# Kernel tuning notes

Measured on AMD Instinct MI355X. Metric: run time of the kernel, lower is better.

The kernel has to match this reference:

```python
import jax, jax.numpy as jnp
import numpy as np

N_HEAD, D_MODEL, D_HEAD = 16, 1024, 64
SEQ, BATCH = 1024, 8
SCALE = 1.0 / (D_HEAD ** 0.5)
LN_EPS = 1e-5


def setup_inputs() -> dict:
    key = jax.random.key(0)
    ks = jax.random.split(key, 16)
    dk = N_HEAD * D_HEAD  # == D_MODEL
    init_qkv = 1.0 / np.sqrt(D_MODEL)
    init_out = 1.0 / np.sqrt(dk)
    u = lambda k, shp, lo, hi: jax.random.uniform(k, shp, jnp.float32, lo, hi)
    inp = {
        'dec_inp': jax.random.normal(ks[0], (SEQ, BATCH, D_MODEL), jnp.float32),
        'attn_mask': jnp.triu(jnp.ones((SEQ, SEQ), dtype=bool), k=1),  # causal
        'query_mean': u(ks[1], (dk, D_MODEL), -init_qkv, init_qkv),
        'key_mean': u(ks[2], (dk, D_MODEL), -init_qkv, init_qkv),
        'value_mean': u(ks[3], (dk, D_MODEL), -init_qkv, init_qkv),
        'query_std': u(ks[4], (dk, D_MODEL), 2 * np.log(init_qkv), np.log(init_qkv)),
        'key_std': u(ks[5], (dk, D_MODEL), 2 * np.log(init_qkv), np.log(init_qkv)),
        'value_std': u(ks[6], (dk, D_MODEL), 2 * np.log(init_qkv), np.log(init_qkv)),
        'output_mean': u(ks[7], (D_MODEL, dk), -init_out, init_out),
        'output_std': u(ks[8], (D_MODEL, dk), 2 * np.log(init_out), np.log(init_out)),
        'ln_gamma': jnp.ones((D_MODEL,), jnp.float32),
        'ln_beta': jnp.zeros((D_MODEL,), jnp.float32),
        # per-forward reparameterization noise (training mode)
        'eps_q': jax.random.normal(ks[9], (dk, D_MODEL), jnp.float32),
        'eps_k': jax.random.normal(ks[10], (dk, D_MODEL), jnp.float32),
        'eps_v': jax.random.normal(ks[11], (dk, D_MODEL), jnp.float32),
        'eps_o': jax.random.normal(ks[12], (D_MODEL, dk), jnp.float32),
    }
    return inp


def _forward(dec_inp, query_mean, key_mean, value_mean, query_std, key_std,
             value_std, output_mean, output_std, ln_gamma, ln_beta,
             eps_q, eps_k, eps_v, eps_o, attn_mask):
    S, B, _ = dec_inp.shape
    # Bayesian weight sampling: w = mean + eps * exp(std)
    qw = query_mean + eps_q * jnp.exp(query_std)
    kw = key_mean + eps_k * jnp.exp(key_std)
    vw = value_mean + eps_v * jnp.exp(value_std)
    # NOTE: original code (bug kept for faithfulness) builds the output weight
    # from value_mean + output_diff, not output_mean.
    ow = value_mean + eps_o * jnp.exp(output_std)

    head_q = (dec_inp @ qw.T).reshape(S, B, N_HEAD, D_HEAD)
    head_k = (dec_inp @ kw.T).reshape(S, B, N_HEAD, D_HEAD)
    head_v = (dec_inp @ vw.T).reshape(S, B, N_HEAD, D_HEAD)

    score = jnp.einsum('ibnd,jbnd->ijbn', head_q, head_k) * SCALE
    score = jnp.where(attn_mask[:, :, None, None], -jnp.inf, score)
    prob = jax.nn.softmax(score, axis=1)  # softmax over j (key) axis
    attn_vec = jnp.einsum('ijbn,jbnd->ibnd', prob, head_v).reshape(S, B, N_HEAD * D_HEAD)

    attn_out = attn_vec @ ow.T
    x = dec_inp + attn_out
    mu = jnp.mean(x, axis=-1, keepdims=True)
    var = jnp.var(x, axis=-1, keepdims=True)
    output = (x - mu) * jax.lax.rsqrt(var + LN_EPS) * ln_gamma + ln_beta

    theta_mean = jnp.concatenate([query_mean, key_mean, value_mean, output_mean.T], -1)
    theta_std = jnp.concatenate([query_std, key_std, value_std, output_std.T], -1)
    kl = jnp.mean(theta_mean ** 2 - theta_std * 2.0 + jnp.exp(theta_std * 2.0)) / 2.0
    return output, kl


def reference(dec_inp, attn_mask, query_mean, key_mean, value_mean, query_std,
              key_std, value_std, output_mean, output_std, ln_gamma, ln_beta,
              eps_q, eps_k, eps_v, eps_o):
    return _forward(dec_inp, query_mean, key_mean, value_mean, query_std,
                    key_std, value_std, output_mean, output_std, ln_gamma,
                    ln_beta, eps_q, eps_k, eps_v, eps_o, attn_mask)
```

## Files before the change

kernel.cpp:

```cpp
#include <hip/hip_runtime.h>

typedef _Float16 f16x8 __attribute__((ext_vector_type(8)));
typedef _Float16 f16x4 __attribute__((ext_vector_type(4)));
typedef float    f32x4 __attribute__((ext_vector_type(4)));

static __device__ __forceinline__ f32x4 mfma16(f16x8 a, f16x8 b, f32x4 c) {
    return __builtin_amdgcn_mfma_f32_16x16x32_f16(a, b, c, 0, 0, 0);
}

static __device__ __forceinline__ void gload_lds16(const _Float16* g, _Float16* lds) {
    __builtin_amdgcn_global_load_lds(
        (const __attribute__((address_space(1))) unsigned int*)g,
        (__attribute__((address_space(3))) unsigned int*)lds, 16, 0, 0);
}

__global__ __launch_bounds__(256) void k_prep(
    const float* __restrict__ qm, const float* __restrict__ km, const float* __restrict__ vm,
    const float* __restrict__ qs, const float* __restrict__ ks, const float* __restrict__ vs,
    const float* __restrict__ om, const float* __restrict__ os,
    const float* __restrict__ eq, const float* __restrict__ ek,
    const float* __restrict__ ev, const float* __restrict__ eo,
    _Float16* __restrict__ wq, _Float16* __restrict__ wk,
    _Float16* __restrict__ wv, _Float16* __restrict__ wo,
    float* __restrict__ part,
    const float* __restrict__ dec, _Float16* __restrict__ xh)
{
    if (blockIdx.x >= 4096) {
        int i = ((blockIdx.x - 4096) * 256 + threadIdx.x) * 4;
        float4 v = *(const float4*)&dec[i];
        f16x4 hv;
        hv[0] = (_Float16)v.x; hv[1] = (_Float16)v.y;
        hv[2] = (_Float16)v.z; hv[3] = (_Float16)v.w;
        *(f16x4*)&xh[i] = hv;
        return;
    }
    int i = blockIdx.x * 256 + threadIdx.x;
    float aqm = qm[i], akm = km[i], avm = vm[i];
    float aqs = qs[i], aks = ks[i], avs = vs[i];
    float aom = om[i], aos = os[i];
    wq[i] = (_Float16)(aqm + eq[i] * __expf(aqs));
    wk[i] = (_Float16)(akm + ek[i] * __expf(aks));
    wv[i] = (_Float16)(avm + ev[i] * __expf(avs));
    wo[i] = (_Float16)(avm + eo[i] * __expf(aos));
    float t = aqm*aqm - 2.f*aqs + __expf(2.f*aqs)
            + akm*akm - 2.f*aks + __expf(2.f*aks)
            + avm*avm - 2.f*avs + __expf(2.f*avs)
            + aom*aom - 2.f*aos + __expf(2.f*aos);
    #pragma unroll
    for (int m = 1; m < 64; m <<= 1) t += __shfl_xor(t, m, 64);
    __shared__ float red[4];
    int w = threadIdx.x >> 6, lane = threadIdx.x & 63;
    if (lane == 0) red[w] = t;
    __syncthreads();
    if (threadIdx.x == 0) part[blockIdx.x] = red[0] + red[1] + red[2] + red[3];
}

__global__ __launch_bounds__(256) void k_gemm(
    const _Float16* __restrict__ A, const _Float16* __restrict__ B0,
    _Float16* __restrict__ C0, const float* __restrict__ resid,
    float* __restrict__ xout, int mode)
{
    __shared__ __align__(16) _Float16 As[128 * 64];
    __shared__ __align__(16) _Float16 Bs[128 * 64];
    const int K = 1024, N = 1024;
    const _Float16* Bp = B0 + (size_t)blockIdx.z * 1048576u;
    _Float16* Cp = C0 + (size_t)blockIdx.z * 8388608u;
    int flat = blockIdx.y * 8 + blockIdx.x;
    int xcd = flat & 7, j = flat >> 3;
    int tM = (xcd * 8 + (j & 7)) * 128;
    int tN = (j >> 3) * 128;
    int tid = threadIdx.x, w = tid >> 6, lane = tid & 63;
    int wm = w & 1, wn = w >> 1;
    int q = lane >> 4, r = lane & 15;
    int csrc = ((lane & 7) ^ (lane >> 3)) * 8;
    int srow = lane >> 3;
    f32x4 acc[4][4] = {};
    for (int kk = 0; kk < K; kk += 64) {
        __syncthreads();
        #pragma unroll
        for (int i = 0; i < 4; ++i) {
            int chunk = w * 4 + i;
            int row = chunk * 8 + srow;
            gload_lds16(A  + (size_t)(tM + row) * K + kk + csrc, &As[chunk * 512]);
            gload_lds16(Bp + (size_t)(tN + row) * K + kk + csrc, &Bs[chunk * 512]);
        }
        __syncthreads();
        #pragma unroll
        for (int kc = 0; kc < 2; ++kc) {
            f16x8 af[4], bf[4];
            #pragma unroll
            for (int m = 0; m < 4; ++m) {
                int row = wm*64 + m*16 + r;
                int pos = ((kc*4 + q) ^ (r & 7)) * 8;
                af[m] = *(const f16x8*)&As[row*64 + pos];
            }
            #pragma unroll
            for (int n = 0; n < 4; ++n) {
                int row = wn*64 + n*16 + r;
                int pos = ((kc*4 + q) ^ (r & 7)) * 8;
                bf[n] = *(const f16x8*)&Bs[row*64 + pos];
            }
            #pragma unroll
            for (int m = 0; m < 4; ++m)
                #pragma unroll
                for (int n = 0; n < 4; ++n)
                    acc[m][n] = mfma16(af[m], bf[n], acc[m][n]);
        }
    }
    float sc = (mode == 0 && blockIdx.z == 0) ? 0.125f : 1.0f;
    #pragma unroll
    for (int m = 0; m < 4; ++m)
      #pragma unroll
      for (int n = 0; n < 4; ++n)
        #pragma unroll
        for (int t = 0; t < 4; ++t) {
            int row = tM + wm*64 + m*16 + q*4 + t;
            int col = tN + wn*64 + n*16 + r;
            size_t o = (size_t)row * N + col;
            if (mode == 0) Cp[o] = (_Float16)(acc[m][n][t] * sc);
            else           xout[o] = resid[o] + acc[m][n][t];
        }
}

__global__ __launch_bounds__(256) void k_vtrans(const _Float16* __restrict__ V,
                                                _Float16* __restrict__ Vt)
{
    __shared__ __align__(16) _Float16 L[64 * 72];
    int c = blockIdx.x;
    int b = c >> 4, h = c & 15;
    int s0 = blockIdx.y * 64;
    int tid = threadIdx.x;
    #pragma unroll
    for (int rep = 0; rep < 2; ++rep) {
        int idx = rep * 256 + tid;
        int sl = idx >> 3, ch = idx & 7;
        f16x8 v = *(const f16x8*)&V[((size_t)(s0 + sl) * 8 + b) * 1024 + h * 64 + ch * 8];
        *(f16x8*)&L[sl * 72 + ch * 8] = v;
    }
    __syncthreads();
    #pragma unroll
    for (int rep = 0; rep < 2; ++rep) {
        int idx = rep * 256 + tid;
        int d = idx >> 3, c2 = idx & 7;
        f16x8 o;
        #pragma unroll
        for (int e = 0; e < 8; ++e) o[e] = L[(c2 * 8 + e) * 72 + d];
        *(f16x8*)&Vt[((size_t)c * 64 + d) * 1024 + s0 + c2 * 8] = o;
    }
}

__global__ __launch_bounds__(256, 4) void k_attn(
    const _Float16* __restrict__ Qb, const _Float16* __restrict__ Kb,
    const _Float16* __restrict__ Vtg, _Float16* __restrict__ AVo)
{
    __shared__ __align__(16) _Float16 Ks[64 * 64];
    __shared__ __align__(16) _Float16 Vs[64 * 64];
    __shared__ __align__(16) _Float16 Ps[4 * 32 * 72];
    const int bh = blockIdx.x;
    const int b = bh & 7, h = bh >> 3;
    const int cbh = b * 16 + h;
    const int qt = blockIdx.y;
    const int tid = threadIdx.x, w = tid >> 6, lane = tid & 63;
    const int q = lane >> 4, r = lane & 15;
    const int i0 = qt * 128 + w * 32;
    const int csrc = ((lane & 7) ^ (lane >> 3)) * 8;
    const int srow = lane >> 3;

    f16x8 qf[2][2];
    #pragma unroll
    for (int it = 0; it < 2; ++it)
      #pragma unroll
      for (int kc = 0; kc < 2; ++kc)
        qf[it][kc] = *(const f16x8*)&Qb[((size_t)(i0 + it*16 + r)*8 + b)*1024 + h*64 + kc*32 + q*8];

    f32x4 ot[4][2] = {};
    float mrun[2] = {-1e30f, -1e30f}, lrun[2] = {0.f, 0.f};
    _Float16* Pw = &Ps[w * 2304];

    auto tile = [&](int kt, bool MASK) __attribute__((always_inline)) {
        __syncthreads();
        #pragma unroll
        for (int ii = 0; ii < 2; ++ii) {
            int chunk = w * 2 + ii;
            int row = chunk * 8 + srow;
            gload_lds16(Kb  + ((size_t)(kt*64 + row)*8 + b)*1024 + h*64 + csrc, &Ks[chunk*512]);
            gload_lds16(Vtg + ((size_t)(cbh*64 + row))*1024 + kt*64 + csrc,     &Vs[chunk*512]);
        }
        __syncthreads();

        f32x4 st[4][2] = {};
        #pragma unroll
        for (int kc = 0; kc < 2; ++kc) {
            f16x8 kf[4];
            #pragma unroll
            for (int jt = 0; jt < 4; ++jt) {
                int pos = ((kc*4 + q) ^ (r & 7)) * 8;
                kf[jt] = *(const f16x8*)&Ks[(jt*16 + r)*64 + pos];
            }
            #pragma unroll
            for (int jt = 0; jt < 4; ++jt)
              #pragma unroll
              for (int it = 0; it < 2; ++it)
                st[jt][it] = mfma16(kf[jt], qf[it][kc], st[jt][it]);
        }

        #pragma unroll
        for (int it = 0; it < 2; ++it) {
            if (MASK) {
                int il = i0 + it*16 + r;
                #pragma unroll
                for (int jt = 0; jt < 4; ++jt)
                  #pragma unroll
                  for (int t = 0; t < 4; ++t)
                    if (kt*64 + jt*16 + q*4 + t > il) st[jt][it][t] = -1e30f;
            }
            float mx = -1e30f;
            #pragma unroll
            for (int jt = 0; jt < 4; ++jt) {
                f32x4 s4 = st[jt][it];
                mx = fmaxf(mx, fmaxf(fmaxf(s4[0], s4[1]), fmaxf(s4[2], s4[3])));
            }
            mx = fmaxf(mx, __shfl_xor(mx, 16, 64));
            mx = fmaxf(mx, __shfl_xor(mx, 32, 64));
            float mnew = fmaxf(mrun[it], mx);
            float al = __expf(mrun[it] - mnew);
            mrun[it] = mnew;
            float ps = 0.f;
            #pragma unroll
            for (int jt = 0; jt < 4; ++jt) {
                f16x4 hv;
                #pragma unroll
                for (int t = 0; t < 4; ++t) {
                    float e = __expf(st[jt][it][t] - mnew);
                    ps += e;
                    hv[t] = (_Float16)e;
                }
                *(f16x4*)&Pw[(it*16 + r)*72 + jt*16 + q*4] = hv;
            }
            ps += __shfl_xor(ps, 16, 64);
            ps += __shfl_xor(ps, 32, 64);
            lrun[it] = lrun[it] * al + ps;
            #pragma unroll
            for (int dtb = 0; dtb < 4; ++dtb) ot[dtb][it] *= al;
        }

        #pragma unroll
        for (int kc = 0; kc < 2; ++kc) {
            f16x8 vf[4], pf[2];
            #pragma unroll
            for (int dtb = 0; dtb < 4; ++dtb) {
                int pos = ((kc*4 + q) ^ (r & 7)) * 8;
                vf[dtb] = *(const f16x8*)&Vs[(dtb*16 + r)*64 + pos];
            }
            #pragma unroll
            for (int it = 0; it < 2; ++it)
                pf[it] = *(const f16x8*)&Pw[(it*16 + r)*72 + kc*32 + q*8];
            #pragma unroll
            for (int dtb = 0; dtb < 4; ++dtb)
              #pragma unroll
              for (int it = 0; it < 2; ++it)
                ot[dtb][it] = mfma16(vf[dtb], pf[it], ot[dtb][it]);
        }
    };

    for (int kt = 0; kt < 2*qt; ++kt) tile(kt, false);
    tile(2*qt,     true);
    tile(2*qt + 1, true);

    #pragma unroll
    for (int it = 0; it < 2; ++it) {
        float inv = 1.f / lrun[it];
        int s = i0 + it*16 + r;
        #pragma unroll
        for (int dtb = 0; dtb < 4; ++dtb) {
            f16x4 hv;
            #pragma unroll
            for (int t = 0; t < 4; ++t) hv[t] = (_Float16)(ot[dtb][it][t] * inv);
            *(f16x4*)&AVo[((size_t)s*8 + b)*1024 + h*64 + dtb*16 + q*4] = hv;
        }
    }
}

__global__ __launch_bounds__(256) void k_ln(float* __restrict__ x,
    const float* __restrict__ g, const float* __restrict__ bta,
    const float* __restrict__ part)
{
    __shared__ float rs[4], rs2[4];
    int w = threadIdx.x >> 6, lane = threadIdx.x & 63;
    if (blockIdx.x == 8192) {
        float s = 0.f;
        for (int i = threadIdx.x; i < 4096; i += 256) s += part[i];
        #pragma unroll
        for (int m = 1; m < 64; m <<= 1) s += __shfl_xor(s, m, 64);
        if (lane == 0) rs[w] = s;
        __syncthreads();
        if (threadIdx.x == 0)
            x[8388608] = (rs[0] + rs[1] + rs[2] + rs[3]) * (0.5f / 4194304.f);
        return;
    }
    int row = blockIdx.x;
    float* xr = x + (size_t)row * 1024;
    int t4 = threadIdx.x * 4;
    float4 v = *(const float4*)&xr[t4];
    float s  = v.x + v.y + v.z + v.w;
    float s2 = v.x*v.x + v.y*v.y + v.z*v.z + v.w*v.w;
    #pragma unroll
    for (int m = 1; m < 64; m <<= 1) { s += __shfl_xor(s, m, 64); s2 += __shfl_xor(s2, m, 64); }
    if (lane == 0) { rs[w] = s; rs2[w] = s2; }
    __syncthreads();
    s  = rs[0] + rs[1] + rs[2] + rs[3];
    s2 = rs2[0] + rs2[1] + rs2[2] + rs2[3];
    float mu = s * (1.f / 1024.f);
    float var = s2 * (1.f / 1024.f) - mu * mu;
    float rstd = rsqrtf(var + 1e-5f);
    float4 gv = *(const float4*)&g[t4];
    float4 bv = *(const float4*)&bta[t4];
    float4 ov;
    ov.x = (v.x - mu) * rstd * gv.x + bv.x;
    ov.y = (v.y - mu) * rstd * gv.y + bv.y;
    ov.z = (v.z - mu) * rstd * gv.z + bv.z;
    ov.w = (v.w - mu) * rstd * gv.w + bv.w;
    *(float4*)&xr[t4] = ov;
}

extern "C" void kernel_launch(void* const* d_in, const int* in_sizes, int n_in,
                              void* d_out, int out_size, void* d_ws, size_t ws_size,
                              hipStream_t stream)
{
    (void)in_sizes; (void)n_in; (void)out_size; (void)ws_size;
    const float* dec   = (const float*)d_in[0];
    const float* qm    = (const float*)d_in[2];
    const float* km    = (const float*)d_in[3];
    const float* vm    = (const float*)d_in[4];
    const float* qs    = (const float*)d_in[5];
    const float* ks    = (const float*)d_in[6];
    const float* vs    = (const float*)d_in[7];
    const float* om    = (const float*)d_in[8];
    const float* os    = (const float*)d_in[9];
    const float* gamma = (const float*)d_in[10];
    const float* beta  = (const float*)d_in[11];
    const float* eq    = (const float*)d_in[12];
    const float* ek    = (const float*)d_in[13];
    const float* ev    = (const float*)d_in[14];
    const float* eo    = (const float*)d_in[15];

    char* ws = (char*)d_ws;
    _Float16* WQ   = (_Float16*)ws;
    float*    PART = (float*)(ws + (8ull  << 20));
    _Float16* XH   = (_Float16*)(ws + (9ull  << 20));
    _Float16* Qh   = (_Float16*)(ws + (25ull << 20));
    _Float16* Kh   = Qh + 8388608;
    _Float16* Vh   = Qh + 16777216;
    _Float16* Vtg  = XH;
    _Float16* AV   = Vh;
    float*    out  = (float*)d_out;

    k_prep<<<dim3(12288), dim3(256), 0, stream>>>(
        qm, km, vm, qs, ks, vs, om, os, eq, ek, ev, eo,
        WQ, WQ + 1048576, WQ + 2097152, WQ + 3145728, PART, dec, XH);
    k_gemm<<<dim3(8, 64, 3), dim3(256), 0, stream>>>(XH, WQ, Qh, dec, out, 0);
    k_vtrans<<<dim3(128, 16), dim3(256), 0, stream>>>(Vh, Vtg);
    k_attn<<<dim3(128, 8), dim3(256), 0, stream>>>(Qh, Kh, Vtg, AV);
    k_gemm<<<dim3(8, 64, 1), dim3(256), 0, stream>>>(AV, WQ + 3145728, Qh, dec, out, 1);
    k_ln<<<dim3(8193), dim3(256), 0, stream>>>(out, gamma, beta, PART);
}
```

Measured before the change: 339.4 us.

## Double-buffer GEMM LDS tiles and fuse V transpose into projection epilogue

The GEMM now keeps two LDS buffers and issues the async global-to-LDS loads for the next K-slice before computing the current one, which removes one barrier per iteration and overlaps loads with MFMA work. The V projection epilogue writes its output directly in the transposed [b,h,d,s] layout, so the separate k_vtrans kernel and its round trip through memory are gone. Workspace buffers are remapped so AV reuses XH. The cost is double the LDS per block, which may reduce occupancy, and strided scalar stores in the transposed epilogue, which coalesce poorly.

```diff
diff --git a/kernel.cpp b/kernel.cpp
--- a/kernel.cpp
+++ b/kernel.cpp
@@ -60,8 +60,8 @@
     _Float16* __restrict__ C0, const float* __restrict__ resid,
     float* __restrict__ xout, int mode)
 {
-    __shared__ __align__(16) _Float16 As[128 * 64];
-    __shared__ __align__(16) _Float16 Bs[128 * 64];
+    __shared__ __align__(16) _Float16 As[2][128 * 64];
+    __shared__ __align__(16) _Float16 Bs[2][128 * 64];
     const int K = 1024, N = 1024;
     const _Float16* Bp = B0 + (size_t)blockIdx.z * 1048576u;
     _Float16* Cp = C0 + (size_t)blockIdx.z * 8388608u;
@@ -74,32 +74,39 @@
     int q = lane >> 4, r = lane & 15;
     int csrc = ((lane & 7) ^ (lane >> 3)) * 8;
     int srow = lane >> 3;
+    const _Float16* Ag = A  + (size_t)tM * K + csrc;
+    const _Float16* Bg = Bp + (size_t)tN * K + csrc;
+
     f32x4 acc[4][4] = {};
+    #pragma unroll
+    for (int i = 0; i < 4; ++i) {
+        int chunk = w * 4 + i;
+        int row = chunk * 8 + srow;
+        gload_lds16(Ag + (size_t)row * K, &As[0][chunk * 512]);
+        gload_lds16(Bg + (size_t)row * K, &Bs[0][chunk * 512]);
+    }
     for (int kk = 0; kk < K; kk += 64) {
+        int cur = (kk >> 6) & 1;
         __syncthreads();
-        #pragma unroll
-        for (int i = 0; i < 4; ++i) {
-            int chunk = w * 4 + i;
-            int row = chunk * 8 + srow;
-            gload_lds16(A  + (size_t)(tM + row) * K + kk + csrc, &As[chunk * 512]);
-            gload_lds16(Bp + (size_t)(tN + row) * K + kk + csrc, &Bs[chunk * 512]);
-        }
-        __syncthreads();
+        if (kk + 64 < K) {
+            #pragma unroll
+            for (int i = 0; i < 4; ++i) {
+                int chunk = w * 4 + i;
+                int row = chunk * 8 + srow;
+                gload_lds16(Ag + (size_t)row * K + kk + 64, &As[cur ^ 1][chunk * 512]);
+                gload_lds16(Bg + (size_t)row * K + kk + 64, &Bs[cur ^ 1][chunk * 512]);
+            }
+        }
         #pragma unroll
         for (int kc = 0; kc < 2; ++kc) {
             f16x8 af[4], bf[4];
-            #pragma unroll
-            for (int m = 0; m < 4; ++m) {
-                int row = wm*64 + m*16 + r;
-                int pos = ((kc*4 + q) ^ (r & 7)) * 8;
-                af[m] = *(const f16x8*)&As[row*64 + pos];
-            }
-            #pragma unroll
-            for (int n = 0; n < 4; ++n) {
-                int row = wn*64 + n*16 + r;
-                int pos = ((kc*4 + q) ^ (r & 7)) * 8;
-                bf[n] = *(const f16x8*)&Bs[row*64 + pos];
-            }
+            int pos = ((kc*4 + q) ^ (r & 7)) * 8;
+            #pragma unroll
+            for (int m = 0; m < 4; ++m)
+                af[m] = *(const f16x8*)&As[cur][(wm*64 + m*16 + r)*64 + pos];
+            #pragma unroll
+            for (int n = 0; n < 4; ++n)
+                bf[n] = *(const f16x8*)&Bs[cur][(wn*64 + n*16 + r)*64 + pos];
             #pragma unroll
             for (int m = 0; m < 4; ++m)
                 #pragma unroll
@@ -108,6 +115,7 @@
         }
     }
     float sc = (mode == 0 && blockIdx.z == 0) ? 0.125f : 1.0f;
+    bool vtr = (mode == 0 && blockIdx.z == 2);
     #pragma unroll
     for (int m = 0; m < 4; ++m)
       #pragma unroll
@@ -116,37 +124,17 @@
         for (int t = 0; t < 4; ++t) {
             int row = tM + wm*64 + m*16 + q*4 + t;
             int col = tN + wn*64 + n*16 + r;
-            size_t o = (size_t)row * N + col;
-            if (mode == 0) Cp[o] = (_Float16)(acc[m][n][t] * sc);
-            else           xout[o] = resid[o] + acc[m][n][t];
-        }
-}
-
-__global__ __launch_bounds__(256) void k_vtrans(const _Float16* __restrict__ V,
-                                                _Float16* __restrict__ Vt)
-{
-    __shared__ __align__(16) _Float16 L[64 * 72];
-    int c = blockIdx.x;
-    int b = c >> 4, h = c & 15;
-    int s0 = blockIdx.y * 64;
-    int tid = threadIdx.x;
-    #pragma unroll
-    for (int rep = 0; rep < 2; ++rep) {
-        int idx = rep * 256 + tid;
-        int sl = idx >> 3, ch = idx & 7;
-        f16x8 v = *(const f16x8*)&V[((size_t)(s0 + sl) * 8 + b) * 1024 + h * 64 + ch * 8];
-        *(f16x8*)&L[sl * 72 + ch * 8] = v;
-    }
-    __syncthreads();
-    #pragma unroll
-    for (int rep = 0; rep < 2; ++rep) {
-        int idx = rep * 256 + tid;
-        int d = idx >> 3, c2 = idx & 7;
-        f16x8 o;
-        #pragma unroll
-        for (int e = 0; e < 8; ++e) o[e] = L[(c2 * 8 + e) * 72 + d];
-        *(f16x8*)&Vt[((size_t)c * 64 + d) * 1024 + s0 + c2 * 8] = o;
-    }
+            if (mode != 0) {
+                size_t o = (size_t)row * N + col;
+                xout[o] = resid[o] + acc[m][n][t];
+            } else if (vtr) {
+                int s = row >> 3, b = row & 7;
+                int h = col >> 6, d = col & 63;
+                Cp[((size_t)((b*16 + h)*64 + d))*1024 + s] = (_Float16)acc[m][n][t];
+            } else {
+                Cp[(size_t)row * N + col] = (_Float16)(acc[m][n][t] * sc);
+            }
+        }
 }
 
 __global__ __launch_bounds__(256, 4) void k_attn(
@@ -350,16 +338,14 @@
     _Float16* XH   = (_Float16*)(ws + (9ull  << 20));
     _Float16* Qh   = (_Float16*)(ws + (25ull << 20));
     _Float16* Kh   = Qh + 8388608;
-    _Float16* Vh   = Qh + 16777216;
-    _Float16* Vtg  = XH;
-    _Float16* AV   = Vh;
+    _Float16* Vtg  = Qh + 16777216;
+    _Float16* AV   = XH;
     float*    out  = (float*)d_out;
 
     k_prep<<<dim3(12288), dim3(256), 0, stream>>>(
         qm, km, vm, qs, ks, vs, om, os, eq, ek, ev, eo,
         WQ, WQ + 1048576, WQ + 2097152, WQ + 3145728, PART, dec, XH);
     k_gemm<<<dim3(8, 64, 3), dim3(256), 0, stream>>>(XH, WQ, Qh, dec, out, 0);
-    k_vtrans<<<dim3(128, 16), dim3(256), 0, stream>>>(Vh, Vtg);
     k_attn<<<dim3(128, 8), dim3(256), 0, stream>>>(Qh, Kh, Vtg, AV);
     k_gemm<<<dim3(8, 64, 1), dim3(256), 0, stream>>>(AV, WQ + 3145728, Qh, dec, out, 1);
     k_ln<<<dim3(8193), dim3(256), 0, stream>>>(out, gamma, beta, PART);
```

Result: slower. 352.3 us (+3.8%).
